# Performance work log

Hardware: AMD Instinct MI355X
Metric: run time of the kernel (lower is better)

## Reference

```python
import jax, jax.numpy as jnp
import numpy as np

G = 128          # voxel grid extent: (range_max - range_min) / voxel_size
N = 100_000      # occupied input voxels (pre-unique)
CIN, COUT = 32, 64
BN_EPS = 1e-5


def _build_positions():
    rng = np.random.default_rng(0)
    pos = rng.integers(0, G, size=(N, 3), dtype=np.int32)
    pos = np.unique(pos, axis=0)  # one feature row per active voxel
    # calculate_grid: offsets (i-2) for i in 0..2 -> {-2,-1,0}^3, filter to [0,G), unique
    offs = np.stack(np.meshgrid(*([np.arange(-2, 1)] * 3), indexing='ij'), -1).reshape(-1, 3)
    op = (pos[:, None, :] + offs[None, :, :]).reshape(-1, 3)
    op = op[(op.min(1) >= 0) & (op.max(1) < G)]
    op = np.unique(op, axis=0)
    return pos.astype(np.int32), op.astype(np.int32)


def setup_inputs() -> dict:
    pos, out_pos = _build_positions()
    key = jax.random.key(0)
    kf, kw = jax.random.split(key)
    n_in = pos.shape[0]
    features = jax.random.normal(kf, (n_in, CIN), dtype=jnp.float32)
    # kaiming-style fan-in init for the 3x3x3 kernel: fan_in = 27 * CIN
    weight = jax.random.normal(kw, (27, CIN, COUT), dtype=jnp.float32) * np.float32(np.sqrt(2.0 / (27 * CIN)))
    gamma = jnp.ones((COUT,), jnp.float32)
    beta = jnp.zeros((COUT,), jnp.float32)
    return {"features": features, "weight": weight, "gamma": gamma, "beta": beta,
            "positions": jnp.asarray(pos), "out_positions": jnp.asarray(out_pos)}


def reference(features, weight, gamma, beta, positions, out_positions):
    n_in, cin = features.shape
    cout = weight.shape[-1]
    # dense coord -> row-index hash grid; pad by 2 since taps reach out_pos + 2
    grid = jnp.full((G + 2, G + 2, G + 2), -1, jnp.int32)
    grid = grid.at[positions[:, 0], positions[:, 1], positions[:, 2]].set(
        jnp.arange(n_in, dtype=jnp.int32))
    # row of zeros for missing neighbors (index -1 wraps to the last row)
    feat_pad = jnp.concatenate([features, jnp.zeros((1, cin), features.dtype)], axis=0)
    ox, oy, oz = out_positions[:, 0], out_positions[:, 1], out_positions[:, 2]
    out = jnp.zeros((out_positions.shape[0], cout), features.dtype)
    k = 0
    # out position o gathers inputs at o + {0,1,2}^3 (mirror of the {-2,-1,0} offsets)
    for dx in range(3):
        for dy in range(3):
            for dz in range(3):
                idx = grid[ox + dx, oy + dy, oz + dz]          # [M] (-1 if empty)
                out = out + feat_pad[idx] @ weight[k]          # [M,Cin]@[Cin,Cout]
                k += 1
    # BatchNorm1d (training mode, stats over all output voxels) + ReLU
    mean = out.mean(axis=0)
    var = out.var(axis=0)
    out = (out - mean) * jax.lax.rsqrt(var + BN_EPS) * gamma + beta
    return jax.nn.relu(out)
```

## Files before the change

### kernel.cpp

```cpp
#include <hip/hip_runtime.h>

#define GD 130
#define GD2 (GD*GD)
#define GRID_ELEMS (GD*GD*GD)
#define STATS_BYTES 1024
#define WPB 16
#define CONV_BLOCKS 256
#define MAX_NIN 100000
#define MAX_NOUT 1600000
#define WSTRIDE 5

typedef _Float16 f16x8 __attribute__((ext_vector_type(8)));
typedef float    f32x16 __attribute__((ext_vector_type(16)));

__device__ _Float16 g_feat16[(MAX_NIN + 1) * 32];
__device__ _Float16 g_out16[(size_t)MAX_NOUT * 64];

__device__ __forceinline__ f32x16 mfma_f16(uint4 a, uint4 b, f32x16 c) {
    union { uint4 u; f16x8 h; } A, B;
    A.u = a; B.u = b;
    return __builtin_amdgcn_mfma_f32_32x32x16_f16(A.h, B.h, c, 0, 0, 0);
}

__global__ __launch_bounds__(256) void scatter_grid_k(
    const int* __restrict__ pos, int* __restrict__ grid, int n_in)
{
    int i = blockIdx.x * blockDim.x + threadIdx.x;
    if (i < n_in) {
        int x = pos[3*i], y = pos[3*i+1], z = pos[3*i+2];
        grid[(x*GD + y)*GD + z] = i;
    }
}

__global__ __launch_bounds__(256) void feat_to_f16_k(
    const float* __restrict__ feat, int n_in)
{
    int i = (blockIdx.x * blockDim.x + threadIdx.x) * 8;
    const int ntot = (n_in + 1) * 32;
    if (i < ntot) {
        union { _Float16 h[8]; uint4 u; } t;
        if (i < n_in * 32) {
            const float4 a = *reinterpret_cast<const float4*>(feat + i);
            const float4 b = *reinterpret_cast<const float4*>(feat + i + 4);
            t.h[0] = (_Float16)a.x; t.h[1] = (_Float16)a.y;
            t.h[2] = (_Float16)a.z; t.h[3] = (_Float16)a.w;
            t.h[4] = (_Float16)b.x; t.h[5] = (_Float16)b.y;
            t.h[6] = (_Float16)b.z; t.h[7] = (_Float16)b.w;
        } else {
            t.u = uint4{0u, 0u, 0u, 0u};
        }
        *reinterpret_cast<uint4*>(g_feat16 + i) = t.u;
    }
}

__global__ __launch_bounds__(1024, 4) void conv_mfma_k(
    const float* __restrict__ W,
    const int* __restrict__ outpos, const int* __restrict__ grid,
    float* __restrict__ stats, int n_out, int n_in)
{
    __shared__ uint4 wlds[27*64*WSTRIDE];
    __shared__ float sstat[128];

    const int tid  = threadIdx.x;
    const int lane = tid & 63;
    const int wid  = tid >> 6;
    const int oc   = lane & 31;
    const int hi   = lane >> 5;

    for (int g = tid; g < 27*64*4; g += 1024) {
        const int k   = g >> 8;
        const int rem = g & 255;
        const int o   = rem >> 2;
        const int q   = rem & 3;
        union { _Float16 h[8]; uint4 u; } t;
        #pragma unroll
        for (int j = 0; j < 8; ++j)
            t.h[j] = (_Float16)W[k*2048 + (q*8 + j)*64 + o];
        wlds[(k*64 + o)*WSTRIDE + q] = t.u;
    }
    if (tid < 128) sstat[tid] = 0.f;
    __syncthreads();

    unsigned* g_o32 = reinterpret_cast<unsigned*>(g_out16);

    const int nchunks = (n_out + 63) >> 6;
    const int xcd  = blockIdx.x & 7;
    const int lw   = (blockIdx.x >> 3) * WPB + wid;
    const int nlw  = (gridDim.x >> 3) * WPB;
    const int Q    = (nchunks + 7) >> 3;
    const int cLo  = xcd * Q;
    const int cHi  = min(cLo + Q, nchunks);

    float ssum0 = 0.f, ssq0 = 0.f, ssum1 = 0.f, ssq1 = 0.f;

    for (int ch = cLo + lw; ch < cHi; ch += nlw) {
        const int r0 = ch << 6;
        const int rb0 = min(r0 + oc,      n_out - 1);
        const int rb1 = min(r0 + 32 + oc, n_out - 1);
        const int x0 = outpos[3*rb0], y0 = outpos[3*rb0+1], z0 = outpos[3*rb0+2];
        const int x1 = outpos[3*rb1], y1 = outpos[3*rb1+1], z1 = outpos[3*rb1+2];
        const int gb0 = (x0*GD + y0)*GD + z0;
        const int gb1 = (x1*GD + y1)*GD + z1;

        f32x16 acc00 = {0.f};
        f32x16 acc01 = {0.f};
        f32x16 acc10 = {0.f};
        f32x16 acc11 = {0.f};

        #pragma unroll
        for (int grp = 0; grp < 3; ++grp) {
            int id0[9], id1[9];
            #pragma unroll
            for (int i = 0; i < 9; ++i) {
                const int t  = grp*9 + i;
                const int dx = t / 9, dyz = t - 9*dx;
                const int dy = dyz / 3, dz = dyz - 3*dy;
                const int off = dx*GD2 + dy*GD + dz;
                id0[i] = grid[gb0 + off];
                id1[i] = grid[gb1 + off];
            }
            #pragma unroll
            for (int i = 0; i < 9; ++i) {
                const int t = grp*9 + i;
                const int wb = (t*64 + oc)*WSTRIDE + hi;
                const uint4 b00 = wlds[wb];
                const uint4 b10 = wlds[wb + 2];
                const uint4 b01 = wlds[wb + 32*WSTRIDE];
                const uint4 b11 = wlds[wb + 32*WSTRIDE + 2];
                {
                    const int s = id0[i] < 0 ? n_in : id0[i];
                    const uint4* fp = reinterpret_cast<const uint4*>(
                        g_feat16 + (size_t)s * 32);
                    const uint4 a0 = fp[hi], a1 = fp[2 + hi];
                    acc00 = mfma_f16(a0, b00, acc00);
                    acc00 = mfma_f16(a1, b10, acc00);
                    acc01 = mfma_f16(a0, b01, acc01);
                    acc01 = mfma_f16(a1, b11, acc01);
                }
                {
                    const int s = id1[i] < 0 ? n_in : id1[i];
                    const uint4* fp = reinterpret_cast<const uint4*>(
                        g_feat16 + (size_t)s * 32);
                    const uint4 a0 = fp[hi], a1 = fp[2 + hi];
                    acc10 = mfma_f16(a0, b00, acc10);
                    acc10 = mfma_f16(a1, b10, acc10);
                    acc11 = mfma_f16(a0, b01, acc11);
                    acc11 = mfma_f16(a1, b11, acc11);
                }
            }
        }

        if (r0 + 64 <= n_out) {
            #pragma unroll
            for (int j = 0; j < 16; ++j) {
                const int rl = (j & 3) + 8*(j >> 2) + 4*hi;
                union { unsigned u; _Float16 h[2]; } p0, p1;
                const float v00 = acc00[j], v01 = acc01[j];
                const float v10 = acc10[j], v11 = acc11[j];
                p0.h[0] = (_Float16)v00; p0.h[1] = (_Float16)v01;
                p1.h[0] = (_Float16)v10; p1.h[1] = (_Float16)v11;
                g_o32[(size_t)(r0 + rl) * 32 + oc]      = p0.u;
                g_o32[(size_t)(r0 + 32 + rl) * 32 + oc] = p1.u;
                ssum0 += v00 + v10; ssq0 = fmaf(v00, v00, fmaf(v10, v10, ssq0));
                ssum1 += v01 + v11; ssq1 = fmaf(v01, v01, fmaf(v11, v11, ssq1));
            }
        } else {
            #pragma unroll
            for (int j = 0; j < 16; ++j) {
                const int rl = (j & 3) + 8*(j >> 2) + 4*hi;
                if (r0 + rl < n_out) {
                    const float v00 = acc00[j], v01 = acc01[j];
                    union { unsigned u; _Float16 h[2]; } p0;
                    p0.h[0] = (_Float16)v00; p0.h[1] = (_Float16)v01;
                    g_o32[(size_t)(r0 + rl) * 32 + oc] = p0.u;
                    ssum0 += v00; ssq0 = fmaf(v00, v00, ssq0);
                    ssum1 += v01; ssq1 = fmaf(v01, v01, ssq1);
                }
                if (r0 + 32 + rl < n_out) {
                    const float v10 = acc10[j], v11 = acc11[j];
                    union { unsigned u; _Float16 h[2]; } p1;
                    p1.h[0] = (_Float16)v10; p1.h[1] = (_Float16)v11;
                    g_o32[(size_t)(r0 + 32 + rl) * 32 + oc] = p1.u;
                    ssum0 += v10; ssq0 = fmaf(v10, v10, ssq0);
                    ssum1 += v11; ssq1 = fmaf(v11, v11, ssq1);
                }
            }
        }
    }

    atomicAdd(&sstat[oc],          ssum0);
    atomicAdd(&sstat[32 + oc],     ssum1);
    atomicAdd(&sstat[64 + oc],     ssq0);
    atomicAdd(&sstat[96 + oc],     ssq1);
    __syncthreads();
    if (tid < 128) unsafeAtomicAdd(&stats[tid], sstat[tid]);
}

__global__ __launch_bounds__(256) void bn_relu_k(
    float* __restrict__ out, const float* __restrict__ stats,
    const float* __restrict__ gamma, const float* __restrict__ beta, int n_out)
{
    __shared__ float sc[64], sh[64];
    if (threadIdx.x < 64) {
        const int c = threadIdx.x;
        const double inv_n = 1.0 / (double)n_out;
        const double mean = (double)stats[c] * inv_n;
        const double var  = (double)stats[64 + c] * inv_n - mean * mean;
        const float scale = gamma[c] * rsqrtf((float)var + 1e-5f);
        sc[c] = scale;
        sh[c] = beta[c] - (float)mean * scale;
    }
    __syncthreads();

    const size_t total8 = (size_t)n_out * 8;
    for (size_t t = (size_t)blockIdx.x * blockDim.x + threadIdx.x;
         t < total8; t += (size_t)gridDim.x * blockDim.x) {
        union { uint4 u; _Float16 h[8]; } v;
        v.u = *reinterpret_cast<const uint4*>(g_out16 + t * 8);
        const int c0 = ((int)(t & 7)) * 4;
        float4 r0, r1;
        r0.x = fmaxf(fmaf((float)v.h[0], sc[c0+0],    sh[c0+0]),    0.f);
        r1.x = fmaxf(fmaf((float)v.h[1], sc[c0+32],   sh[c0+32]),   0.f);
        r0.y = fmaxf(fmaf((float)v.h[2], sc[c0+1],    sh[c0+1]),    0.f);
        r1.y = fmaxf(fmaf((float)v.h[3], sc[c0+33],   sh[c0+33]),   0.f);
        r0.z = fmaxf(fmaf((float)v.h[4], sc[c0+2],    sh[c0+2]),    0.f);
        r1.z = fmaxf(fmaf((float)v.h[5], sc[c0+34],   sh[c0+34]),   0.f);
        r0.w = fmaxf(fmaf((float)v.h[6], sc[c0+3],    sh[c0+3]),    0.f);
        r1.w = fmaxf(fmaf((float)v.h[7], sc[c0+35],   sh[c0+35]),   0.f);
        float* rowp = out + (size_t)(t >> 3) * 64;
        *reinterpret_cast<float4*>(rowp + c0)      = r0;
        *reinterpret_cast<float4*>(rowp + 32 + c0) = r1;
    }
}

extern "C" void kernel_launch(void* const* d_in, const int* in_sizes, int n_in_arrs,
                              void* d_out, int out_size, void* d_ws, size_t ws_size,
                              hipStream_t stream)
{
    const float* feat   = (const float*)d_in[0];
    const float* W      = (const float*)d_in[1];
    const float* gamma  = (const float*)d_in[2];
    const float* beta   = (const float*)d_in[3];
    const int*   pos    = (const int*)d_in[4];
    const int*   outpos = (const int*)d_in[5];

    const int n_in  = in_sizes[0] / 32;
    const int n_out = in_sizes[5] / 3;

    float* out   = (float*)d_out;
    float* stats = (float*)d_ws;
    int*   grid  = (int*)((char*)d_ws + STATS_BYTES);

    hipMemsetAsync(stats, 0, STATS_BYTES, stream);
    hipMemsetAsync(grid, 0xFF, (size_t)GRID_ELEMS * 4, stream);

    scatter_grid_k<<<(n_in + 255) / 256, 256, 0, stream>>>(pos, grid, n_in);
    feat_to_f16_k<<<((n_in + 1) * 4 + 255) / 256, 256, 0, stream>>>(feat, n_in);
    conv_mfma_k<<<CONV_BLOCKS, 1024, 0, stream>>>(W, outpos, grid, stats, n_out, n_in);
    bn_relu_k<<<2048, 256, 0, stream>>>(out, stats, gamma, beta, n_out);
}
```

Before: 361.0 us.

## Vectorize grid probes, prefetch next row, skip taps with empty neighbors

Replaces the 27 scalar hash-grid lookups per output row with 9 unaligned 16-byte loads along z, each prefetched one step ahead. Adds wave-wide ballots so that MFMA work and feature gathers are skipped for a tap or half-tile when no lane in the wave has an occupied neighbor. The memset grows by four ints to cover the overread past the grid end. This risks misaligned vector loads and extra branching, and the skip only helps when whole waves see empty taps, which depends on how sparse the data is.

```diff
diff --git a/kernel.cpp b/kernel.cpp
--- a/kernel.cpp
+++ b/kernel.cpp
@@ -53,6 +53,12 @@
     }
 }
 
+__device__ __forceinline__ int4 probe4(const int* __restrict__ grid, int base) {
+    int4 p;
+    __builtin_memcpy(&p, grid + base, 16);
+    return p;
+}
+
 __global__ __launch_bounds__(1024, 4) void conv_mfma_k(
     const float* __restrict__ W,
     const int* __restrict__ outpos, const int* __restrict__ grid,
@@ -97,38 +103,43 @@
         const int r0 = ch << 6;
         const int rb0 = min(r0 + oc,      n_out - 1);
         const int rb1 = min(r0 + 32 + oc, n_out - 1);
-        const int x0 = outpos[3*rb0], y0 = outpos[3*rb0+1], z0 = outpos[3*rb0+2];
-        const int x1 = outpos[3*rb1], y1 = outpos[3*rb1+1], z1 = outpos[3*rb1+2];
-        const int gb0 = (x0*GD + y0)*GD + z0;
-        const int gb1 = (x1*GD + y1)*GD + z1;
+        int3 c0, c1;
+        __builtin_memcpy(&c0, outpos + 3*rb0, 12);
+        __builtin_memcpy(&c1, outpos + 3*rb1, 12);
+        const int gb0 = (c0.x*GD + c0.y)*GD + c0.z;
+        const int gb1 = (c1.x*GD + c1.y)*GD + c1.z;
 
         f32x16 acc00 = {0.f};
         f32x16 acc01 = {0.f};
         f32x16 acc10 = {0.f};
         f32x16 acc11 = {0.f};
 
+        int4 p0c = probe4(grid, gb0);
+        int4 p1c = probe4(grid, gb1);
+        int4 p0n, p1n;
+
         #pragma unroll
-        for (int grp = 0; grp < 3; ++grp) {
-            int id0[9], id1[9];
+        for (int g = 0; g < 9; ++g) {
+            if (g < 8) {
+                const int off = ((g+1)/3)*GD2 + ((g+1)%3)*GD;
+                p0n = probe4(grid, gb0 + off);
+                p1n = probe4(grid, gb1 + off);
+            }
+            const int id0[3] = { p0c.x, p0c.y, p0c.z };
+            const int id1[3] = { p1c.x, p1c.y, p1c.z };
             #pragma unroll
-            for (int i = 0; i < 9; ++i) {
-                const int t  = grp*9 + i;
-                const int dx = t / 9, dyz = t - 9*dx;
-                const int dy = dyz / 3, dz = dyz - 3*dy;
-                const int off = dx*GD2 + dy*GD + dz;
-                id0[i] = grid[gb0 + off];
-                id1[i] = grid[gb1 + off];
-            }
-            #pragma unroll
-            for (int i = 0; i < 9; ++i) {
-                const int t = grp*9 + i;
+            for (int dz = 0; dz < 3; ++dz) {
+                const unsigned long long mA = __ballot(id0[dz] >= 0);
+                const unsigned long long mB = __ballot(id1[dz] >= 0);
+                if (!(mA | mB)) continue;
+                const int t = g*3 + dz;
                 const int wb = (t*64 + oc)*WSTRIDE + hi;
                 const uint4 b00 = wlds[wb];
                 const uint4 b10 = wlds[wb + 2];
                 const uint4 b01 = wlds[wb + 32*WSTRIDE];
                 const uint4 b11 = wlds[wb + 32*WSTRIDE + 2];
-                {
-                    const int s = id0[i] < 0 ? n_in : id0[i];
+                if (mA) {
+                    const int s = id0[dz] < 0 ? n_in : id0[dz];
                     const uint4* fp = reinterpret_cast<const uint4*>(
                         g_feat16 + (size_t)s * 32);
                     const uint4 a0 = fp[hi], a1 = fp[2 + hi];
@@ -137,8 +148,8 @@
                     acc01 = mfma_f16(a0, b01, acc01);
                     acc01 = mfma_f16(a1, b11, acc01);
                 }
-                {
-                    const int s = id1[i] < 0 ? n_in : id1[i];
+                if (mB) {
+                    const int s = id1[dz] < 0 ? n_in : id1[dz];
                     const uint4* fp = reinterpret_cast<const uint4*>(
                         g_feat16 + (size_t)s * 32);
                     const uint4 a0 = fp[hi], a1 = fp[2 + hi];
@@ -148,19 +159,20 @@
                     acc11 = mfma_f16(a1, b11, acc11);
                 }
             }
+            p0c = p0n; p1c = p1n;
         }
 
         if (r0 + 64 <= n_out) {
             #pragma unroll
             for (int j = 0; j < 16; ++j) {
                 const int rl = (j & 3) + 8*(j >> 2) + 4*hi;
-                union { unsigned u; _Float16 h[2]; } p0, p1;
+                union { unsigned u; _Float16 h[2]; } q0, q1;
                 const float v00 = acc00[j], v01 = acc01[j];
                 const float v10 = acc10[j], v11 = acc11[j];
-                p0.h[0] = (_Float16)v00; p0.h[1] = (_Float16)v01;
-                p1.h[0] = (_Float16)v10; p1.h[1] = (_Float16)v11;
-                g_o32[(size_t)(r0 + rl) * 32 + oc]      = p0.u;
-                g_o32[(size_t)(r0 + 32 + rl) * 32 + oc] = p1.u;
+                q0.h[0] = (_Float16)v00; q0.h[1] = (_Float16)v01;
+                q1.h[0] = (_Float16)v10; q1.h[1] = (_Float16)v11;
+                g_o32[(size_t)(r0 + rl) * 32 + oc]      = q0.u;
+                g_o32[(size_t)(r0 + 32 + rl) * 32 + oc] = q1.u;
                 ssum0 += v00 + v10; ssq0 = fmaf(v00, v00, fmaf(v10, v10, ssq0));
                 ssum1 += v01 + v11; ssq1 = fmaf(v01, v01, fmaf(v11, v11, ssq1));
             }
@@ -170,17 +182,17 @@
                 const int rl = (j & 3) + 8*(j >> 2) + 4*hi;
                 if (r0 + rl < n_out) {
                     const float v00 = acc00[j], v01 = acc01[j];
-                    union { unsigned u; _Float16 h[2]; } p0;
-                    p0.h[0] = (_Float16)v00; p0.h[1] = (_Float16)v01;
-                    g_o32[(size_t)(r0 + rl) * 32 + oc] = p0.u;
+                    union { unsigned u; _Float16 h[2]; } q0;
+                    q0.h[0] = (_Float16)v00; q0.h[1] = (_Float16)v01;
+                    g_o32[(size_t)(r0 + rl) * 32 + oc] = q0.u;
                     ssum0 += v00; ssq0 = fmaf(v00, v00, ssq0);
                     ssum1 += v01; ssq1 = fmaf(v01, v01, ssq1);
                 }
                 if (r0 + 32 + rl < n_out) {
                     const float v10 = acc10[j], v11 = acc11[j];
-                    union { unsigned u; _Float16 h[2]; } p1;
-                    p1.h[0] = (_Float16)v10; p1.h[1] = (_Float16)v11;
-                    g_o32[(size_t)(r0 + 32 + rl) * 32 + oc] = p1.u;
+                    union { unsigned u; _Float16 h[2]; } q1;
+                    q1.h[0] = (_Float16)v10; q1.h[1] = (_Float16)v11;
+                    g_o32[(size_t)(r0 + 32 + rl) * 32 + oc] = q1.u;
                     ssum0 += v10; ssq0 = fmaf(v10, v10, ssq0);
                     ssum1 += v11; ssq1 = fmaf(v11, v11, ssq1);
                 }
@@ -252,7 +264,7 @@
     int*   grid  = (int*)((char*)d_ws + STATS_BYTES);
 
     hipMemsetAsync(stats, 0, STATS_BYTES, stream);
-    hipMemsetAsync(grid, 0xFF, (size_t)GRID_ELEMS * 4, stream);
+    hipMemsetAsync(grid, 0xFF, ((size_t)GRID_ELEMS + 4) * 4, stream);
 
     scatter_grid_k<<<(n_in + 255) / 256, 256, 0, stream>>>(pos, grid, n_in);
     feat_to_f16_k<<<((n_in + 1) * 4 + 255) / 256, 256, 0, stream>>>(feat, n_in);
```

After: 363.5 us. Within noise of the previous version (+0.7%).
